# Kernel tuning notes

Hardware: AMD Instinct MI355X
Metric: run time of the kernel (lower is better)

## Reference

```python
import jax, jax.numpy as jnp
import numpy as np

B, X, Y, Z = 2, 64, 64, 48
T_IN, T_OUT = 10, 20
WIDTH = 20
G = 4              # number of fields / groups
M1 = M2 = M3 = 8   # fourier modes
L = 4              # layers
ORDER = [[0, 1, 2, 3], [1, 2, 3, 0], [2, 3, 0, 1], [3, 0, 1, 2]]
CIN = WIDTH * 4    # mWidth_input_parameters[i] == 4
COUT = WIDTH       # nWidth_output_parameters[i] == 1
EPS = 1e-5


def setup_inputs() -> dict:
    key = jax.random.key(0)
    ks = jax.random.split(key, 12)
    s = 0.02
    return {
        "x": jax.random.normal(ks[0], (B, X, Y, Z, G * T_IN), jnp.float32),
        "p_w": jax.random.normal(ks[1], (G, T_IN + 3, WIDTH), jnp.float32) * s,
        "p_b": jnp.zeros((G, WIDTH), jnp.float32),
        # complex spectral weights stored as (..., 2) = (real, imag); 4 corner blocks
        "spec_w": jax.random.normal(ks[2], (L, G, 4, CIN, COUT, M1, M2, M3, 2), jnp.float32) * (1.0 / CIN),
        "mlp_w1": jax.random.normal(ks[3], (L, G, COUT, COUT), jnp.float32) * s,
        "mlp_b1": jnp.zeros((L, G, COUT), jnp.float32),
        "mlp_w2": jax.random.normal(ks[4], (L, G, COUT, COUT), jnp.float32) * s,
        "mlp_b2": jnp.zeros((L, G, COUT), jnp.float32),
        "w_w": jax.random.normal(ks[5], (L, G, COUT, CIN), jnp.float32) * s,
        "w_b": jnp.zeros((L, G, COUT), jnp.float32),
        "q_w1": jax.random.normal(ks[6], (G, 4 * COUT, COUT), jnp.float32) * s,
        "q_b1": jnp.zeros((G, 4 * COUT), jnp.float32),
        "q_w2": jax.random.normal(ks[7], (G, T_OUT, 4 * COUT), jnp.float32) * s,
        "q_b2": jnp.zeros((G, T_OUT), jnp.float32),
    }


def _instance_norm(v):  # (B,C,X,Y,Z); InstanceNorm3d, affine=False
    m = v.mean(axis=(-3, -2, -1), keepdims=True)
    var = v.var(axis=(-3, -2, -1), keepdims=True)
    return (v - m) * jax.lax.rsqrt(var + EPS)


def _conv1x1(v, w, b):  # w: (Co, Ci)
    return jnp.einsum('bixyz,oi->boxyz', v, w) + b[None, :, None, None, None]


def _gelu(v):
    return jax.nn.gelu(v, approximate=False)


def _spectral(v, w):  # v: (B,Ci,X,Y,Z); w: complex (4,Ci,Co,M1,M2,M3)
    ft = jnp.fft.rfftn(v, axes=(-3, -2, -1))
    mul = lambda xc, wc: jnp.einsum('bixyz,ioxyz->boxyz', xc, wc)
    out = jnp.zeros((v.shape[0], w.shape[2], X, Y, Z // 2 + 1), ft.dtype)
    out = out.at[:, :, :M1, :M2, :M3].set(mul(ft[:, :, :M1, :M2, :M3], w[0]))
    out = out.at[:, :, -M1:, :M2, :M3].set(mul(ft[:, :, -M1:, :M2, :M3], w[1]))
    out = out.at[:, :, :M1, -M2:, :M3].set(mul(ft[:, :, :M1, -M2:, :M3], w[2]))
    out = out.at[:, :, -M1:, -M2:, :M3].set(mul(ft[:, :, -M1:, -M2:, :M3], w[3]))
    return jnp.fft.irfftn(out, s=(X, Y, Z), axes=(-3, -2, -1))


def _grid():  # (1,X,Y,Z,3), linspace 0..1 per axis
    gx = jnp.linspace(0.0, 1.0, X, dtype=jnp.float32)[:, None, None]
    gy = jnp.linspace(0.0, 1.0, Y, dtype=jnp.float32)[None, :, None]
    gz = jnp.linspace(0.0, 1.0, Z, dtype=jnp.float32)[None, None, :]
    g = jnp.stack([jnp.broadcast_to(gx, (X, Y, Z)),
                   jnp.broadcast_to(gy, (X, Y, Z)),
                   jnp.broadcast_to(gz, (X, Y, Z))], axis=-1)
    return g[None]


def reference(x, p_w, p_b, spec_w, mlp_w1, mlp_b1, mlp_w2, mlp_b2,
              w_w, w_b, q_w1, q_b1, q_w2, q_b2):
    grid = jnp.broadcast_to(_grid(), (x.shape[0], X, Y, Z, 3))
    # --- lifting: per-field Linear(T_in+3 -> width) ---
    lifted = [jnp.concatenate([x[..., i * T_IN:(i + 1) * T_IN], grid], axis=-1) @ p_w[i] + p_b[i]
              for i in range(G)]
    h = jnp.concatenate(lifted, axis=-1).transpose(0, 4, 1, 2, 3)  # (B, width*G, X, Y, Z)
    sw = spec_w[..., 0] + 1j * spec_w[..., 1]
    for l in range(L):
        for i in range(G):
            # faithful gather quirk: first index duplicated, last index dropped
            idx = [ORDER[i][0]] + ORDER[i][:-1]
            xg = jnp.concatenate([h[:, WIDTH * k:WIDTH * (k + 1)] for k in idx], axis=1)
            v = _instance_norm(xg)
            v = _spectral(v, sw[l, i])
            v = _instance_norm(v)
            v = _conv1x1(_gelu(_conv1x1(v, mlp_w1[l, i], mlp_b1[l, i])), mlp_w2[l, i], mlp_b2[l, i])
            r = _conv1x1(xg, w_w[l, i], w_b[l, i])
            h = h.at[:, WIDTH * i:WIDTH * (i + 1)].set(v + r)
        if l != L - 1:
            h = _gelu(h)
    # --- projection: per-field MLP (T_OUT == WIDTH so slices align to field blocks) ---
    outs = []
    for i in range(G):
        lo = (WIDTH if i == 0 else T_OUT) * i
        xi = h[:, lo:lo + WIDTH]
        xi = _conv1x1(_gelu(_conv1x1(xi, q_w1[i], q_b1[i])), q_w2[i], q_b2[i])
        outs.append(xi)
    out = jnp.concatenate(outs, axis=1)
    return out.transpose(0, 2, 3, 4, 1)  # (B,X,Y,Z,G*T_OUT)
```

## Files before the change

### kernel.cpp

```cpp
#include <hip/hip_runtime.h>
#include <math.h>

#define SPAT 196608
#define EPSV 1e-5f

__device__ __forceinline__ float geluf(float x){
    float ax = fabsf(x)*0.70710678118654752440f;
    float t = __builtin_amdgcn_rcpf(1.0f + 0.3275911f*ax);
    float p = ((((1.061405429f*t - 1.453152027f)*t + 1.421413741f)*t - 0.284496736f)*t + 0.254829592f)*t;
    float e = 1.0f - p*__expf(-ax*ax);
    float er = copysignf(e, x);
    return 0.5f*x*(1.0f + er);
}
__device__ __forceinline__ float wred(float v){
    #pragma unroll
    for(int o=32;o>0;o>>=1) v += __shfl_down(v,o);
    return v;
}

__global__ void k_tables(float* tab){
    for(int idx=threadIdx.x; idx<384; idx+=blockDim.x){
        int z = idx>>3, k = idx&7;
        double a = 6.283185307179586476925286766559 * (double)((k*z)%48) / 48.0;
        float c = (float)cos(a), s = (float)sin(a);
        tab[idx]=c; tab[384+idx]=s;
        tab[768 + k*48+z]=c; tab[1152 + k*48+z]=s;
    }
    for(int idx=threadIdx.x; idx<1024; idx+=blockDim.x){
        int y = idx>>4, ki = idx&15;
        int ka = ki<8 ? ki : ki+48;
        double a = 6.283185307179586476925286766559 * (double)((ka*y)%64) / 64.0;
        float c=(float)cos(a), s=(float)sin(a);
        tab[1536+idx]=c; tab[2560+idx]=s;
        tab[3584 + ki*64+y]=c; tab[4608 + ki*64+y]=s;
    }
}

__global__ void __launch_bounds__(256) k_lift(const float* __restrict__ x,
                       const float* __restrict__ pw, const float* __restrict__ pb,
                       float* __restrict__ h){
    int t = blockIdx.x*256 + threadIdx.x;
    int b = (t>=SPAT) ? 1 : 0; int col = t - b*SPAT;
    int xy = col/48, z = col%48;
    const float4* xp = (const float4*)(x + (size_t)t*40);
    float in[40];
    #pragma unroll
    for(int q=0;q<10;q++){
        float4 v = xp[q];
        in[q*4]=v.x; in[q*4+1]=v.y; in[q*4+2]=v.z; in[q*4+3]=v.w;
    }
    float gx = (float)(xy>>6)*(1.0f/63.0f);
    float gy = (float)(xy&63)*(1.0f/63.0f);
    float gz = (float)z*(1.0f/47.0f);
    for(int g=0;g<4;g++){
        const float* w = pw + g*260;
        #pragma unroll 4
        for(int c=0;c<20;c++){
            float a = pb[g*20+c];
            #pragma unroll
            for(int j=0;j<10;j++) a += in[g*10+j]*w[j*20+c];
            a += gx*w[200+c] + gy*w[220+c] + gz*w[240+c];
            h[(size_t)(b*80+g*20+c)*SPAT + col] = a;
        }
    }
}

__global__ void __launch_bounds__(256) k_zy(const float* __restrict__ h,
        float* __restrict__ ybuf, float* __restrict__ partZY,
        const float* __restrict__ tab, int gA,int gB,int gC,int gD, int gflag){
    __shared__ float sp4[4*16*65];
    __shared__ float cyl[16*65], syl[16*65];
    __shared__ float sred[8];
    int blk = blockIdx.x;
    int x = blk&63; int d=(blk>>6)%20; int r2 = blk/1280; int b = r2&1; int gi = r2>>1;
    int gl4[4]={gA,gB,gC,gD};
    int g = gl4[gi];
    int ch = g*20+d;
    int tid=threadIdx.x;
    int y = tid&63, q4 = tid>>6;
    const float4* src = (const float4*)(h + (size_t)(b*80+ch)*SPAT + (size_t)x*3072
                                          + (size_t)(y*48 + q4*12));
    float v[12];
    #pragma unroll
    for(int u=0;u<3;u++){
        float4 t4 = src[u];
        v[u*4]=t4.x; v[u*4+1]=t4.y; v[u*4+2]=t4.z; v[u*4+3]=t4.w;
    }
    if(gflag){
        #pragma unroll
        for(int j=0;j<12;j++) v[j]=geluf(v[j]);
    }
    float s1=0,s2=0;
    #pragma unroll
    for(int j=0;j<12;j++){ s1+=v[j]; s2+=v[j]*v[j]; }
    for(int tt=tid;tt<1024;tt+=256){
        int ki=tt>>6, yy=tt&63;
        cyl[ki*65+yy]=tab[3584+tt]; syl[ki*65+yy]=tab[4608+tt];
    }
    const float* CZ = tab+768  + q4*12;
    const float* SZ = tab+1152 + q4*12;
    #pragma unroll
    for(int k=0;k<8;k++){
        float rr=0, si=0;
        #pragma unroll
        for(int j=0;j<12;j++){ rr += v[j]*CZ[k*48+j]; si += v[j]*SZ[k*48+j]; }
        sp4[(q4*16 + k*2)*65 + y]   = rr;
        sp4[(q4*16 + k*2+1)*65 + y] = -si;
    }
    s1=wred(s1); s2=wred(s2);
    if((tid&63)==0){ sred[(tid>>6)*2]=s1; sred[(tid>>6)*2+1]=s2; }
    __syncthreads();
    if(tid==0){
        size_t pi = ((size_t)(b*80+ch)*64+x)*2;
        partZY[pi]   = sred[0]+sred[2]+sred[4]+sred[6];
        partZY[pi+1] = sred[1]+sred[3]+sred[5]+sred[7];
    }
    #pragma unroll
    for(int j=0;j<4;j++){
        int e = tid + j*256;
        int kri = e>>6, yy = e&63;
        float sum = sp4[kri*65+yy] + sp4[(16+kri)*65+yy]
                  + sp4[(32+kri)*65+yy] + sp4[(48+kri)*65+yy];
        sp4[kri*65+yy] = sum;
    }
    __syncthreads();
    if(tid<128){
        int ky=tid>>3, kz=tid&7;
        const float* cy = cyl+ky*65; const float* sy = syl+ky*65;
        const float* spr = sp4 + (kz*2)*65;
        const float* spi = sp4 + (kz*2+1)*65;
        float fr=0, fi=0;
        #pragma unroll 8
        for(int yy=0;yy<64;yy++){
            float sr=spr[yy], si=spi[yy];
            float c=cy[yy], s=sy[yy];
            fr += sr*c + si*s;
            fi += si*c - sr*s;
        }
        size_t base = ((size_t)((g*2+b)*20+d)*16 + ky)*1024 + (size_t)(kz*128);
        ybuf[base + x]      = fr;
        ybuf[base + 64 + x] = fi;
    }
}

__global__ void __launch_bounds__(128) k_xdft(const float* __restrict__ ybuf,
        float* __restrict__ fbufC, const float* __restrict__ partZY,
        const float* __restrict__ tab, int gA,int gB,int gC,int gD){
    __shared__ __align__(16) float ylx[16*68];
    __shared__ float cxl[16*65], sxl[16*65];
    __shared__ float scs[1];
    int blk = blockIdx.x;
    int kyi = blk&15; int d=(blk>>4)%20; int r2=blk/320; int b=r2&1; int gi=r2>>1;
    int gl4[4]={gA,gB,gC,gD};
    int g=gl4[gi]; int ch=g*20+d;
    int tid=threadIdx.x;
    const float4* src = (const float4*)(ybuf + (((size_t)((g*2+b)*20+d)*16+kyi)*1024));
    #pragma unroll
    for(int u=0;u<2;u++){
        int e=tid+u*128; float4 v=src[e];
        int kzri = e>>4; int xx=(e&15)*4;
        *(float4*)(ylx + kzri*68 + xx) = v;
    }
    for(int tt=tid;tt<1024;tt+=128){
        int ki=tt>>6, y=tt&63;
        cxl[ki*65+y]=tab[3584+tt]; sxl[ki*65+y]=tab[4608+tt];
    }
    float s1=0,s2=0;
    if(tid<64){
        size_t pi=((size_t)(b*80+ch)*64+tid)*2;
        s1=partZY[pi]; s2=partZY[pi+1];
    }
    s1=wred(s1); s2=wred(s2);
    if(tid==0){
        float mean=s1*(1.0f/196608.0f);
        float var=s2*(1.0f/196608.0f)-mean*mean;
        scs[0]=rsqrtf(var+EPSV);
    }
    __syncthreads();
    float sc = scs[0];
    int kxi=tid>>3, kz=tid&7;
    const float* yr = ylx + (kz*2)*68;
    const float* yi = ylx + (kz*2+1)*68;
    const float* cx = cxl + kxi*65;
    const float* sx = sxl + kxi*65;
    float fr=0, fi=0;
    #pragma unroll 8
    for(int xx=0;xx<64;xx++){
        float a=yr[xx], e2=yi[xx];
        float c=cx[xx], s=sx[xx];
        fr += a*c + e2*s;
        fi += e2*c - a*s;
    }
    fr*=sc; fi*=sc;
    if(kxi==0 && kyi==0 && kz==0){ fr=0.0f; fi=0.0f; }
    size_t idx = ((size_t)(b*80+ch)*2048 + (size_t)((kxi*16+kyi)*8+kz))*2;
    fbufC[idx]=fr; fbufC[idx+1]=fi;
}

__global__ void __launch_bounds__(256) k_spec2(const float* __restrict__ fbufC,
        const float* __restrict__ sw, float* __restrict__ gbuf,
        float* __restrict__ stat2, int li0,
        int i0, int gA1, int gA2, int i1, int gB1, int gB2){
    __shared__ float part[2112];
    int blk = blockIdx.x;
    int it = blk/320; int r = blk - it*320;
    int m1p = r & 3, o = (r>>2)%20, q = r/80;
    int li = li0 + it;
    int g0 = it ? i1 : i0;
    int g1 = it ? gB1 : gA1;
    int g2 = it ? gB2 : gA2;
    int tid = threadIdx.x;
    int t64 = tid & 63, cc = tid >> 6;
    if(q==0 && m1p==0 && tid<2){
        stat2[((it*2+tid)*20+o)*2]=0.f; stat2[((it*2+tid)*20+o)*2+1]=0.f;
    }
    int offx = (q&1)*8, offy = (q>>1)*8;
    int m1 = m1p*2 + (t64>>5);
    int m2 = (t64>>2)&7;
    int m3 = (t64&3)*2;
    int tw = m1*64 + m2*8 + m3;
    int kxi = m1+offx, kyi = m2+offy;
    int fo = (kxi*16 + kyi)*8 + m3;
    const float4* wp = (const float4*)(sw + (((size_t)(li*4+q)*1600) + o)*1024 + (size_t)tw*2);
    const float4* fb = (const float4*)fbufC + (fo>>1);
    float r00=0,i00=0,r01=0,i01=0, r10=0,i10=0,r11=0,i11=0;
    int c0 = cc*5;
    #pragma unroll
    for(int u=0;u<5;u++){
        int c = c0+u;
        float4 wa = wp[(size_t)c*5120];
        float4 wb4= wp[(size_t)(c+20)*5120];
        float wr0 = wa.x + wb4.x, wi0 = wa.y + wb4.y, wr1 = wa.z + wb4.z, wi1 = wa.w + wb4.w;
        float4 f0 = fb[(size_t)(g0*20+c)*1024];
        float4 f1 = fb[(size_t)(80+g0*20+c)*1024];
        r00 += f0.x*wr0 - f0.y*wi0; i00 += f0.x*wi0 + f0.y*wr0;
        r01 += f0.z*wr1 - f0.w*wi1; i01 += f0.z*wi1 + f0.w*wr1;
        r10 += f1.x*wr0 - f1.y*wi0; i10 += f1.x*wi0 + f1.y*wr0;
        r11 += f1.z*wr1 - f1.w*wi1; i11 += f1.z*wi1 + f1.w*wr1;
    }
    #pragma unroll
    for(int u=0;u<5;u++){
        int c = c0+u;
        float4 wa = wp[(size_t)(c+40)*5120];
        float4 f0 = fb[(size_t)(g1*20+c)*1024];
        float4 f1 = fb[(size_t)(80+g1*20+c)*1024];
        r00 += f0.x*wa.x - f0.y*wa.y; i00 += f0.x*wa.y + f0.y*wa.x;
        r01 += f0.z*wa.z - f0.w*wa.w; i01 += f0.z*wa.w + f0.w*wa.z;
        r10 += f1.x*wa.x - f1.y*wa.y; i10 += f1.x*wa.y + f1.y*wa.x;
        r11 += f1.z*wa.z - f1.w*wa.w; i11 += f1.z*wa.w + f1.w*wa.z;
    }
    #pragma unroll
    for(int u=0;u<5;u++){
        int c = c0+u;
        float4 wa = wp[(size_t)(c+60)*5120];
        float4 f0 = fb[(size_t)(g2*20+c)*1024];
        float4 f1 = fb[(size_t)(80+g2*20+c)*1024];
        r00 += f0.x*wa.x - f0.y*wa.y; i00 += f0.x*wa.y + f0.y*wa.x;
        r01 += f0.z*wa.z - f0.w*wa.w; i01 += f0.z*wa.w + f0.w*wa.z;
        r10 += f1.x*wa.x - f1.y*wa.y; i10 += f1.x*wa.y + f1.y*wa.x;
        r11 += f1.z*wa.z - f1.w*wa.w; i11 += f1.z*wa.w + f1.w*wa.z;
    }
    float vals[8]={r00,i00,r01,i01,r10,i10,r11,i11};
    #pragma unroll
    for(int e=0;e<8;e++) part[t64*33 + e*4 + cc] = vals[e];
    __syncthreads();
    if(cc==0){
        float acc[8];
        #pragma unroll
        for(int e=0;e<8;e++){
            const float* p = part + t64*33 + e*4;
            acc[e] = p[0]+p[1]+p[2]+p[3];
        }
        float* gb = gbuf + (size_t)it*163840;
        float4* gg0 = (float4*)(gb + (size_t)o*4096 + fo*2);
        float4* gg1 = (float4*)(gb + (size_t)(20+o)*4096 + fo*2);
        *gg0 = make_float4(acc[0],acc[1],acc[2],acc[3]);
        *gg1 = make_float4(acc[4],acc[5],acc[6],acc[7]);
    }
}

__global__ void k_inv2(const float* __restrict__ gbuf, float* __restrict__ iybuf,
                       float* __restrict__ stat2, const float* __restrict__ tab){
    __shared__ __align__(16) float gl[4096];
    __shared__ float tmp[256];
    __shared__ float cl[1088], sl[1088];
    __shared__ float ig[4];
    int blk = blockIdx.x;
    int it = blk/2560; int r = blk - it*2560;
    int nx = r&63, o = (r>>6)%20, b = r/1280;
    const float4* src4 = (const float4*)(gbuf + (size_t)it*163840 + (size_t)(b*20+o)*4096);
    for(int t=threadIdx.x;t<1024;t+=blockDim.x) ((float4*)gl)[t]=src4[t];
    for(int t=threadIdx.x;t<1024;t+=blockDim.x){
        int y=t>>4, ki=t&15;
        cl[y*17+ki]=tab[1536+t]; sl[y*17+ki]=tab[2560+t];
    }
    __syncthreads();
    {
        int kyi = threadIdx.x>>3, kz = threadIdx.x&7;
        float ar=0, ai=0;
        #pragma unroll 4
        for(int kxi=0;kxi<16;kxi++){
            float gr = gl[((kxi*16+kyi)*8+kz)*2], gi2 = gl[((kxi*16+kyi)*8+kz)*2+1];
            float c = cl[nx*17+kxi], s = sl[nx*17+kxi];
            ar += gr*c - gi2*s;
            ai += gi2*c + gr*s;
        }
        tmp[threadIdx.x*2]   = ar*(1.0f/64.0f);
        tmp[threadIdx.x*2+1] = ai*(1.0f/64.0f);
    }
    __syncthreads();
    float p1=0,p2=0;
    for(int j=0;j<4;j++){
        int out = threadIdx.x + j*128;
        int ny = out>>3, kz = out&7;
        float ar=0, ai=0;
        #pragma unroll 4
        for(int kyi=0;kyi<16;kyi++){
            float vr = tmp[(kyi*8+kz)*2], vi = tmp[(kyi*8+kz)*2+1];
            float c = cl[ny*17+kyi], s = sl[ny*17+kyi];
            ar += vr*c - vi*s;
            ai += vi*c + vr*s;
        }
        ar *= (1.0f/64.0f); ai *= (1.0f/64.0f);
        size_t idx = ((((size_t)((it*2+b)*20+o)*64+nx)*64+ny)*8+kz)*2;
        iybuf[idx]=ar; iybuf[idx+1]=ai;
        if(kz==0){ p1 += ar; p2 += ar*ar; }
        else p2 += 2.0f*(ar*ar+ai*ai);
    }
    p2 *= (1.0f/48.0f);
    float r1=wred(p1), r2=wred(p2);
    int wv = threadIdx.x>>6;
    if((threadIdx.x&63)==0){ ig[wv*2]=r1; ig[wv*2+1]=r2; }
    __syncthreads();
    if(threadIdx.x==0){
        atomicAdd(&stat2[((it*2+b)*20+o)*2],   ig[0]+ig[2]);
        atomicAdd(&stat2[((it*2+b)*20+o)*2+1], ig[1]+ig[3]);
    }
}

__global__ void __launch_bounds__(256) k_passD2(
        const float* __restrict__ iybuf,
        const float* __restrict__ w1, const float* __restrict__ b1,
        const float* __restrict__ w2, const float* __restrict__ b2,
        const float* __restrict__ ww, const float* __restrict__ wb,
        float* __restrict__ h,
        const float* __restrict__ stat2, const float* __restrict__ tab,
        int li0, int i0, int i1, int gA1, int gA2, int gB1, int gB2,
        int fA0,int fA1,int fA2, int fB0,int fB1,int fB2){
    __shared__ __align__(16) float dl[5120];
    __shared__ float m2l[2][20], s2l[2][20];
    __shared__ float czl[384], szl[384];
    int blk = blockIdx.x;
    int nyt = blk&7, nx=(blk>>3)&63, b = blk>>9;
    int tid = threadIdx.x;
    for(int u=tid; u<1280; u+=256){
        int itu = (u>=640)?1:0; int rem = u - itu*640;
        int o = rem>>5, j = rem&31;
        const float4* s4 = (const float4*)(iybuf +
            ((((size_t)((itu*2+b)*20+o)*64+nx)*64 + nyt*8)*16));
        ((float4*)dl)[itu*640 + o*32 + j] = s4[j];
    }
    if(tid<40){
        int itq = tid/20, oq = tid - itq*20;
        float S1 = stat2[((itq*2+b)*20+oq)*2], S2 = stat2[((itq*2+b)*20+oq)*2+1];
        float mean = S1*(1.0f/196608.0f);
        float var = S2*(1.0f/196608.0f) - mean*mean;
        m2l[itq][oq]=mean; s2l[itq][oq]=rsqrtf(var+EPSV);
    }
    for(int t=tid;t<384;t+=256){ czl[t]=tab[768+t]; szl[t]=tab[1152+t]; }
    __syncthreads();
    if(tid>=192) return;
    int p0 = tid*2;
    int nyl = p0/48, nz0 = p0 - nyl*48;
    int sb = (nx*64 + nyt*8)*48;
    const float* hb = h + (size_t)(b*80)*SPAT + sb + p0;
    {
        float vj0[20], vj1[20];
        #pragma unroll
        for(int o=0;o<20;o++){
            const float* dd = dl + o*128 + nyl*16;
            float a0 = dd[0], a1 = dd[0];
            #pragma unroll
            for(int k=1;k<8;k++){
                float dr = dd[k*2], di = dd[k*2+1];
                a0 += 2.0f*(dr*czl[k*48+nz0]   - di*szl[k*48+nz0]);
                a1 += 2.0f*(dr*czl[k*48+nz0+1] - di*szl[k*48+nz0+1]);
            }
            vj0[o] = (a0*(1.0f/48.0f) - m2l[0][o])*s2l[0][o];
            vj1[o] = (a1*(1.0f/48.0f) - m2l[0][o])*s2l[0][o];
        }
        const float* W1 = w1 + li0*400; const float* W2 = w2 + li0*400;
        const float* B1 = b1 + li0*20;  const float* B2 = b2 + li0*20;
        float t10[20], t11[20];
        #pragma unroll
        for(int oo=0;oo<20;oo++){
            float a0=B1[oo], a1=a0;
            #pragma unroll
            for(int j=0;j<20;j++){ float w=W1[oo*20+j]; a0+=vj0[j]*w; a1+=vj1[j]*w; }
            t10[oo]=geluf(a0); t11[oo]=geluf(a1);
        }
        float o0[20], o1[20];
        #pragma unroll
        for(int oo=0;oo<20;oo++){
            float bb = B2[oo] + wb[li0*20+oo];
            float a0=bb, a1=bb;
            #pragma unroll
            for(int j=0;j<20;j++){ float w=W2[oo*20+j]; a0+=t10[j]*w; a1+=t11[j]*w; }
            o0[oo]=a0; o1[oo]=a1;
        }
        const float* W = ww + li0*1600;
        for(int c=0;c<20;c++){
            float2 vv = *(const float2*)(hb + (size_t)(i0*20+c)*SPAT);
            if(fA0){ vv.x=geluf(vv.x); vv.y=geluf(vv.y); }
            #pragma unroll
            for(int o=0;o<20;o++){
                float w = W[o*80+c] + W[o*80+20+c];
                o0[o]+=w*vv.x; o1[o]+=w*vv.y;
            }
        }
        for(int c=0;c<20;c++){
            float2 vv = *(const float2*)(hb + (size_t)(gA1*20+c)*SPAT);
            if(fA1){ vv.x=geluf(vv.x); vv.y=geluf(vv.y); }
            #pragma unroll
            for(int o=0;o<20;o++){
                float w = W[o*80+40+c];
                o0[o]+=w*vv.x; o1[o]+=w*vv.y;
            }
        }
        for(int c=0;c<20;c++){
            float2 vv = *(const float2*)(hb + (size_t)(gA2*20+c)*SPAT);
            if(fA2){ vv.x=geluf(vv.x); vv.y=geluf(vv.y); }
            #pragma unroll
            for(int o=0;o<20;o++){
                float w = W[o*80+60+c];
                o0[o]+=w*vv.x; o1[o]+=w*vv.y;
            }
        }
        #pragma unroll
        for(int o=0;o<20;o++)
            *(float2*)(h + (size_t)(b*80+i0*20+o)*SPAT + sb + p0) = make_float2(o0[o],o1[o]);
    }
    {
        int li1 = li0+1;
        float vj0[20], vj1[20];
        #pragma unroll
        for(int o=0;o<20;o++){
            const float* dd = dl + 2560 + o*128 + nyl*16;
            float a0 = dd[0], a1 = dd[0];
            #pragma unroll
            for(int k=1;k<8;k++){
                float dr = dd[k*2], di = dd[k*2+1];
                a0 += 2.0f*(dr*czl[k*48+nz0]   - di*szl[k*48+nz0]);
                a1 += 2.0f*(dr*czl[k*48+nz0+1] - di*szl[k*48+nz0+1]);
            }
            vj0[o] = (a0*(1.0f/48.0f) - m2l[1][o])*s2l[1][o];
            vj1[o] = (a1*(1.0f/48.0f) - m2l[1][o])*s2l[1][o];
        }
        const float* W1 = w1 + li1*400; const float* W2 = w2 + li1*400;
        const float* B1 = b1 + li1*20;  const float* B2 = b2 + li1*20;
        float t10[20], t11[20];
        #pragma unroll
        for(int oo=0;oo<20;oo++){
            float a0=B1[oo], a1=a0;
            #pragma unroll
            for(int j=0;j<20;j++){ float w=W1[oo*20+j]; a0+=vj0[j]*w; a1+=vj1[j]*w; }
            t10[oo]=geluf(a0); t11[oo]=geluf(a1);
        }
        float o0[20], o1[20];
        #pragma unroll
        for(int oo=0;oo<20;oo++){
            float bb = B2[oo] + wb[li1*20+oo];
            float a0=bb, a1=bb;
            #pragma unroll
            for(int j=0;j<20;j++){ float w=W2[oo*20+j]; a0+=t10[j]*w; a1+=t11[j]*w; }
            o0[oo]=a0; o1[oo]=a1;
        }
        const float* W = ww + li1*1600;
        for(int c=0;c<20;c++){
            float2 vv = *(const float2*)(hb + (size_t)(i1*20+c)*SPAT);
            if(fB0){ vv.x=geluf(vv.x); vv.y=geluf(vv.y); }
            #pragma unroll
            for(int o=0;o<20;o++){
                float w = W[o*80+c] + W[o*80+20+c];
                o0[o]+=w*vv.x; o1[o]+=w*vv.y;
            }
        }
        for(int c=0;c<20;c++){
            float2 vv = *(const float2*)(hb + (size_t)(gB1*20+c)*SPAT);
            if(fB1){ vv.x=geluf(vv.x); vv.y=geluf(vv.y); }
            #pragma unroll
            for(int o=0;o<20;o++){
                float w = W[o*80+40+c];
                o0[o]+=w*vv.x; o1[o]+=w*vv.y;
            }
        }
        for(int c=0;c<20;c++){
            float2 vv = *(const float2*)(hb + (size_t)(gB2*20+c)*SPAT);
            if(fB2){ vv.x=geluf(vv.x); vv.y=geluf(vv.y); }
            #pragma unroll
            for(int o=0;o<20;o++){
                float w = W[o*80+60+c];
                o0[o]+=w*vv.x; o1[o]+=w*vv.y;
            }
        }
        #pragma unroll
        for(int o=0;o<20;o++)
            *(float2*)(h + (size_t)(b*80+i1*20+o)*SPAT + sb + p0) = make_float2(o0[o],o1[o]);
    }
}

__global__ void __launch_bounds__(256) k_head(const float* __restrict__ h,
        const float* __restrict__ qw1, const float* __restrict__ qb1,
        const float* __restrict__ qw2, const float* __restrict__ qb2,
        float* __restrict__ out){
    int g = blockIdx.x & 3;
    int t = (blockIdx.x>>2)*256 + threadIdx.x;
    if(t >= 196608) return;
    int b = (t>=98304) ? 1 : 0; int col = (t - b*98304)*2;
    const float* hb = h + (size_t)(b*80+g*20)*SPAT + col;
    float2 in20[20];
    #pragma unroll
    for(int j=0;j<20;j++) in20[j] = *(const float2*)(hb + (size_t)j*SPAT);
    float2 o20[20];
    #pragma unroll
    for(int o2=0;o2<20;o2++){ float bv = qb2[g*20+o2]; o20[o2].x=bv; o20[o2].y=bv; }
    for(int o8=0;o8<80;o8++){
        float bv = qb1[g*80+o8];
        float a0 = bv, a1 = bv;
        #pragma unroll
        for(int j=0;j<20;j++){
            float w = qw1[g*1600 + o8*20 + j];
            a0 += in20[j].x*w; a1 += in20[j].y*w;
        }
        a0 = geluf(a0); a1 = geluf(a1);
        #pragma unroll
        for(int o2=0;o2<20;o2++){
            float w = qw2[g*1600 + o2*80 + o8];
            o20[o2].x += a0*w; o20[o2].y += a1*w;
        }
    }
    float* op0 = out + ((size_t)(b*SPAT)+col)*80 + g*20;
    float* op1 = op0 + 80;
    #pragma unroll
    for(int q2=0;q2<5;q2++){
        *(float4*)(op0 + q2*4) = make_float4(o20[q2*4].x,o20[q2*4+1].x,o20[q2*4+2].x,o20[q2*4+3].x);
        *(float4*)(op1 + q2*4) = make_float4(o20[q2*4].y,o20[q2*4+1].y,o20[q2*4+2].y,o20[q2*4+3].y);
    }
}

extern "C" void kernel_launch(void* const* d_in, const int* in_sizes, int n_in,
                              void* d_out, int out_size, void* d_ws, size_t ws_size,
                              hipStream_t stream){
    (void)in_sizes; (void)n_in; (void)out_size;
    const float* x    = (const float*)d_in[0];
    const float* p_w  = (const float*)d_in[1];
    const float* p_b  = (const float*)d_in[2];
    const float* spec = (const float*)d_in[3];
    const float* w1   = (const float*)d_in[4];
    const float* b1   = (const float*)d_in[5];
    const float* w2   = (const float*)d_in[6];
    const float* b2   = (const float*)d_in[7];
    const float* ww   = (const float*)d_in[8];
    const float* wb   = (const float*)d_in[9];
    const float* qw1  = (const float*)d_in[10];
    const float* qb1  = (const float*)d_in[11];
    const float* qw2  = (const float*)d_in[12];
    const float* qb2  = (const float*)d_in[13];
    float* out = (float*)d_out;
    float* ws  = (float*)d_ws;

    if(ws_size < (size_t)40330912*4) return;

    float* h      = ws;
    float* ybuf   = ws + 31457280;
    float* gbuf   = ws + 34078720;
    float* iyb    = ws + 34406400;
    float* fbufC  = ws + 39649280;
    float* partZY = ws + 40304640;
    float* stat2  = ws + 40325120;
    float* tab    = ws + 40325280;

    k_tables<<<1,256,0,stream>>>(tab);
    k_lift<<<1536,256,0,stream>>>(x, p_w, p_b, h);

    static const int ORD3[4][3] = {{0,1,2},{1,2,3},{2,3,0},{3,0,1}};
    for(int l=0;l<4;l++){
        int lf = (l>0)?1:0;
        for(int bi=0;bi<2;bi++){
            if(bi==0){
                k_zy  <<<10240,256,0,stream>>>(h, ybuf, partZY, tab, 0,1,2,3, lf);
                k_xdft<<< 2560,128,0,stream>>>(ybuf, fbufC, partZY, tab, 0,1,2,3);
            } else {
                k_zy  <<< 5120,256,0,stream>>>(h, ybuf, partZY, tab, 0,1,0,0, 0);
                k_xdft<<< 1280,128,0,stream>>>(ybuf, fbufC, partZY, tab, 0,1,0,0);
            }
            int i0 = bi*2, i1 = i0+1, li0 = l*4+i0;
            int gA1=ORD3[i0][1], gA2=ORD3[i0][2];
            int gB1=ORD3[i1][1], gB2=ORD3[i1][2];
            k_spec2<<< 640,256,0,stream>>>(fbufC, spec, gbuf, stat2, li0,
                                           i0,gA1,gA2, i1,gB1,gB2);
            k_inv2 <<<5120,128,0,stream>>>(gbuf, iyb, stat2, tab);
            int fA0 = lf;
            int fA1 = (gA1<i0)?0:lf;
            int fA2 = (gA2<i0)?0:lf;
            int fB0 = lf;
            int fB1 = (gB1<i1)?0:lf;
            int fB2 = (gB2<i1)?0:lf;
            k_passD2<<<1024,256,0,stream>>>(iyb, w1,b1,w2,b2, ww,wb, h, stat2, tab,
                                            li0, i0,i1, gA1,gA2, gB1,gB2,
                                            fA0,fA1,fA2, fB0,fB1,fB2);
        }
    }
    k_head<<<3072,256,0,stream>>>(h, qw1, qb1, qw2, qb2, out);
}
```

Measured before the change: 3.011 ms.

## Split DFT reductions across threads, pad shared memory, and trim passD2 block size

k_zy now spreads the final y-DFT reduction over all 256 threads, with two halves combined through shared memory, instead of leaving half the block idle. k_inv2 pads its shared spectrum buffer to avoid bank conflicts, switching from float4 to scalar loads. k_passD2 launches 192 threads to match the threads that actually compute, removing the early exit. k_head splits the first-layer dot product into two accumulator chains to shorten the dependency chain. The risks are an extra barrier in k_zy and narrower global loads in k_inv2.

```diff
diff --git a/kernel.cpp b/kernel.cpp
--- a/kernel.cpp
+++ b/kernel.cpp
@@ -71,6 +71,7 @@
     __shared__ float sp4[4*16*65];
     __shared__ float cyl[16*65], syl[16*65];
     __shared__ float sred[8];
+    __shared__ float comb[256];
     int blk = blockIdx.x;
     int x = blk&63; int d=(blk>>6)%20; int r2 = blk/1280; int b = r2&1; int gi = r2>>1;
     int gl4[4]={gA,gB,gC,gD};
@@ -124,22 +125,30 @@
         sp4[kri*65+yy] = sum;
     }
     __syncthreads();
-    if(tid<128){
-        int ky=tid>>3, kz=tid&7;
-        const float* cy = cyl+ky*65; const float* sy = syl+ky*65;
-        const float* spr = sp4 + (kz*2)*65;
-        const float* spi = sp4 + (kz*2+1)*65;
+    {
+        int task = tid & 127;
+        int half = tid >> 7;
+        int ky = task>>3, kz = task&7;
+        const float* cy  = cyl + ky*65 + half*32;
+        const float* sy  = syl + ky*65 + half*32;
+        const float* spr = sp4 + (kz*2)*65 + half*32;
+        const float* spi = sp4 + (kz*2+1)*65 + half*32;
         float fr=0, fi=0;
         #pragma unroll 8
-        for(int yy=0;yy<64;yy++){
+        for(int yy=0;yy<32;yy++){
             float sr=spr[yy], si=spi[yy];
             float c=cy[yy], s=sy[yy];
             fr += sr*c + si*s;
             fi += si*c - sr*s;
         }
-        size_t base = ((size_t)((g*2+b)*20+d)*16 + ky)*1024 + (size_t)(kz*128);
-        ybuf[base + x]      = fr;
-        ybuf[base + 64 + x] = fi;
+        if(half){ comb[task*2]=fr; comb[task*2+1]=fi; }
+        __syncthreads();
+        if(!half){
+            fr += comb[task*2]; fi += comb[task*2+1];
+            size_t base = ((size_t)((g*2+b)*20+d)*16 + ky)*1024 + (size_t)(kz*128);
+            ybuf[base + x]      = fr;
+            ybuf[base + 64 + x] = fi;
+        }
     }
 }
 
@@ -281,15 +290,15 @@
 
 __global__ void k_inv2(const float* __restrict__ gbuf, float* __restrict__ iybuf,
                        float* __restrict__ stat2, const float* __restrict__ tab){
-    __shared__ __align__(16) float gl[4096];
+    __shared__ float gl[4224];
     __shared__ float tmp[256];
     __shared__ float cl[1088], sl[1088];
     __shared__ float ig[4];
     int blk = blockIdx.x;
     int it = blk/2560; int r = blk - it*2560;
     int nx = r&63, o = (r>>6)%20, b = r/1280;
-    const float4* src4 = (const float4*)(gbuf + (size_t)it*163840 + (size_t)(b*20+o)*4096);
-    for(int t=threadIdx.x;t<1024;t+=blockDim.x) ((float4*)gl)[t]=src4[t];
+    const float* srcf = gbuf + (size_t)it*163840 + (size_t)(b*20+o)*4096;
+    for(int t=threadIdx.x;t<4096;t+=blockDim.x) gl[t + (t>>5)] = srcf[t];
     for(int t=threadIdx.x;t<1024;t+=blockDim.x){
         int y=t>>4, ki=t&15;
         cl[y*17+ki]=tab[1536+t]; sl[y*17+ki]=tab[2560+t];
@@ -300,7 +309,9 @@
         float ar=0, ai=0;
         #pragma unroll 4
         for(int kxi=0;kxi<16;kxi++){
-            float gr = gl[((kxi*16+kyi)*8+kz)*2], gi2 = gl[((kxi*16+kyi)*8+kz)*2+1];
+            int v = ((kxi*16+kyi)*8+kz)*2;
+            int pv = v + (v>>5);
+            float gr = gl[pv], gi2 = gl[pv+1];
             float c = cl[nx*17+kxi], s = sl[nx*17+kxi];
             ar += gr*c - gi2*s;
             ai += gi2*c + gr*s;
@@ -338,7 +349,7 @@
     }
 }
 
-__global__ void __launch_bounds__(256) k_passD2(
+__global__ void __launch_bounds__(192) k_passD2(
         const float* __restrict__ iybuf,
         const float* __restrict__ w1, const float* __restrict__ b1,
         const float* __restrict__ w2, const float* __restrict__ b2,
@@ -353,7 +364,7 @@
     int blk = blockIdx.x;
     int nyt = blk&7, nx=(blk>>3)&63, b = blk>>9;
     int tid = threadIdx.x;
-    for(int u=tid; u<1280; u+=256){
+    for(int u=tid; u<1280; u+=192){
         int itu = (u>=640)?1:0; int rem = u - itu*640;
         int o = rem>>5, j = rem&31;
         const float4* s4 = (const float4*)(iybuf +
@@ -367,9 +378,8 @@
         float var = S2*(1.0f/196608.0f) - mean*mean;
         m2l[itq][oq]=mean; s2l[itq][oq]=rsqrtf(var+EPSV);
     }
-    for(int t=tid;t<384;t+=256){ czl[t]=tab[768+t]; szl[t]=tab[1152+t]; }
-    __syncthreads();
-    if(tid>=192) return;
+    for(int t=tid;t<384;t+=192){ czl[t]=tab[768+t]; szl[t]=tab[1152+t]; }
+    __syncthreads();
     int p0 = tid*2;
     int nyl = p0/48, nz0 = p0 - nyl*48;
     int sb = (nx*64 + nyt*8)*48;
@@ -526,13 +536,18 @@
     for(int o2=0;o2<20;o2++){ float bv = qb2[g*20+o2]; o20[o2].x=bv; o20[o2].y=bv; }
     for(int o8=0;o8<80;o8++){
         float bv = qb1[g*80+o8];
-        float a0 = bv, a1 = bv;
-        #pragma unroll
-        for(int j=0;j<20;j++){
+        float a0=bv, a1=bv, c0=0.0f, c1=0.0f;
+        #pragma unroll
+        for(int j=0;j<10;j++){
             float w = qw1[g*1600 + o8*20 + j];
             a0 += in20[j].x*w; a1 += in20[j].y*w;
         }
-        a0 = geluf(a0); a1 = geluf(a1);
+        #pragma unroll
+        for(int j=10;j<20;j++){
+            float w = qw1[g*1600 + o8*20 + j];
+            c0 += in20[j].x*w; c1 += in20[j].y*w;
+        }
+        a0 = geluf(a0+c0); a1 = geluf(a1+c1);
         #pragma unroll
         for(int o2=0;o2<20;o2++){
             float w = qw2[g*1600 + o2*80 + o8];
@@ -606,7 +621,7 @@
             int fB0 = lf;
             int fB1 = (gB1<i1)?0:lf;
             int fB2 = (gB2<i1)?0:lf;
-            k_passD2<<<1024,256,0,stream>>>(iyb, w1,b1,w2,b2, ww,wb, h, stat2, tab,
+            k_passD2<<<1024,192,0,stream>>>(iyb, w1,b1,w2,b2, ww,wb, h, stat2, tab,
                                             li0, i0,i1, gA1,gA2, gB1,gB2,
                                             fA0,fA1,fA2, fB0,fB1,fB2);
         }
```

After: 3.122 ms. 3.7% more time.
